# Kernel tuning notes

Measured on AMD Instinct MI355X. Metric: run time of the kernel, lower is better.

## Reference

```python
import jax, jax.numpy as jnp
import numpy as np

DIM = 192; HEADS = 6; WS = 7; RES = 56; SHIFT = 3
HEAD_DIM = DIM // HEADS
SCALE = HEAD_DIM ** -0.5
N = WS * WS
EPS = 1e-5

def _rel_pos_index():
    coords = np.stack(np.meshgrid(np.arange(WS), np.arange(WS), indexing='ij')).reshape(2, -1)
    rel = coords[:, :, None] - coords[:, None, :]  # [2,N,N]
    rel = rel.transpose(1, 2, 0)
    rel[:, :, 0] += WS - 1
    rel[:, :, 1] += WS - 1
    rel[:, :, 0] *= 2 * WS - 1
    return rel.sum(-1)  # [N,N]

def _attn_mask():
    img = np.zeros((RES, RES), dtype=np.float32)
    slices = (slice(0, -WS), slice(-WS, -SHIFT), slice(-SHIFT, None))
    cnt = 0
    for h in slices:
        for w in slices:
            img[h, w] = cnt; cnt += 1
    mw = img.reshape(RES // WS, WS, RES // WS, WS).transpose(0, 2, 1, 3).reshape(-1, N)  # [nW,N]
    diff = mw[:, None, :] - mw[:, :, None]
    return np.where(diff != 0, -100.0, 0.0).astype(np.float32)  # [nW,N,N]

REL_IDX = jnp.asarray(_rel_pos_index())
ATTN_MASK = jnp.asarray(_attn_mask())

def _ln(x, g, b):
    mu = x.mean(-1, keepdims=True)
    var = ((x - mu) ** 2).mean(-1, keepdims=True)
    return (x - mu) * jax.lax.rsqrt(var + EPS) * g + b

def setup_inputs() -> dict:
    key = jax.random.key(0)
    ks = jax.random.split(key, 8)
    d = {
        'x': jax.random.normal(ks[0], (32, RES * RES, DIM), jnp.float32),
        'norm1_g': jnp.ones((DIM,), jnp.float32), 'norm1_b': jnp.zeros((DIM,), jnp.float32),
        'qkv_w': jax.random.normal(ks[1], (DIM, 3 * DIM), jnp.float32) * 0.02,
        'qkv_b': jnp.zeros((3 * DIM,), jnp.float32),
        'proj_w': jax.random.normal(ks[2], (DIM, DIM), jnp.float32) * 0.02,
        'proj_b': jnp.zeros((DIM,), jnp.float32),
        'bias_table': jax.random.normal(ks[3], ((2 * WS - 1) ** 2, HEADS), jnp.float32) * 0.02,
        'norm2_g': jnp.ones((DIM,), jnp.float32), 'norm2_b': jnp.zeros((DIM,), jnp.float32),
        'fc1_w': jax.random.normal(ks[4], (DIM, 4 * DIM), jnp.float32) * 0.02,
        'fc1_b': jnp.zeros((4 * DIM,), jnp.float32),
        'fc2_w': jax.random.normal(ks[5], (4 * DIM, DIM), jnp.float32) * 0.02,
        'fc2_b': jnp.zeros((DIM,), jnp.float32),
    }
    return d

def reference(x, norm1_g, norm1_b, qkv_w, qkv_b, proj_w, proj_b, bias_table,
              norm2_g, norm2_b, fc1_w, fc1_b, fc2_w, fc2_b):
    B, L, C = x.shape
    H = W = RES
    shortcut = x
    h = _ln(x, norm1_g, norm1_b).reshape(B, H, W, C)
    # cyclic shift
    h = jnp.roll(h, (-SHIFT, -SHIFT), axis=(1, 2))
    # window partition -> [B*nW, N, C]
    nH = H // WS
    h = h.reshape(B, nH, WS, nH, WS, C).transpose(0, 1, 3, 2, 4, 5).reshape(-1, N, C)
    BW = h.shape[0]
    # windowed MHSA
    qkv = (h @ qkv_w + qkv_b).reshape(BW, N, 3, HEADS, HEAD_DIM)
    q, k, v = qkv[:, :, 0], qkv[:, :, 1], qkv[:, :, 2]  # [BW,N,h,hd]
    attn = jnp.einsum('bnhd,bmhd->bhnm', q, k) * SCALE  # [BW,h,N,N]
    bias = bias_table[REL_IDX.reshape(-1)].reshape(N, N, HEADS).transpose(2, 0, 1)
    attn = attn + bias[None]
    nW = ATTN_MASK.shape[0]
    attn = attn.reshape(BW // nW, nW, HEADS, N, N) + ATTN_MASK[None, :, None]
    attn = jax.nn.softmax(attn.reshape(BW, HEADS, N, N), axis=-1)
    h = jnp.einsum('bhnm,bmhd->bnhd', attn, v).reshape(BW, N, C)
    h = h @ proj_w + proj_b
    # window reverse
    h = h.reshape(B, nH, nH, WS, WS, C).transpose(0, 1, 3, 2, 4, 5).reshape(B, H, W, C)
    h = jnp.roll(h, (SHIFT, SHIFT), axis=(1, 2)).reshape(B, L, C)
    x = shortcut + h
    # MLP
    m = _ln(x, norm2_g, norm2_b)
    m = jax.nn.gelu(m @ fc1_w + fc1_b, approximate=False) @ fc2_w + fc2_b
    return x + m
```

## Files before the change

### kernel.cpp

```cpp
#include <hip/hip_runtime.h>
#include <hip/hip_bf16.h>
#include <math.h>

typedef __attribute__((ext_vector_type(8))) short bh8;
typedef __attribute__((ext_vector_type(4))) float fx4;

__device__ __forceinline__ fx4 mfma_bf16(bh8 a, bh8 b, fx4 c) {
    return __builtin_amdgcn_mfma_f32_16x16x32_bf16(a, b, c, 0, 0, 0);
}

__device__ __forceinline__ void gload16(const __hip_bfloat16* g, __hip_bfloat16* l) {
    __builtin_amdgcn_global_load_lds(
        (const __attribute__((address_space(1))) void*)g,
        (__attribute__((address_space(3))) void*)l,
        16, 0, 0);
}

__global__ __launch_bounds__(256)
void convw_k(const float* __restrict__ W, __hip_bfloat16* __restrict__ Wt, int K, int Nn)
{
    int idx = blockIdx.x * 256 + threadIdx.x;
    if (idx < K * Nn) {
        int k = idx / Nn, n = idx - k * Nn;
        Wt[(size_t)n * K + k] = __float2bfloat16(W[idx]);
    }
}

__global__ __launch_bounds__(256)
void ln1_gather_k(const float* __restrict__ x, const float* __restrict__ g,
                  const float* __restrict__ bia, __hip_bfloat16* __restrict__ xw)
{
    const int wave = threadIdx.x >> 6, lane = threadIdx.x & 63;
    const int t = blockIdx.x * 4 + wave;
    const int w = t / 49, n = t - w * 49;
    const int b = w >> 6, wrem = w & 63, wi = wrem >> 3, wj = wrem & 7;
    const int i = n / 7, j = n - i * 7;
    int sr = wi * 7 + i + 3; if (sr >= 56) sr -= 56;
    int sc = wj * 7 + j + 3; if (sc >= 56) sc -= 56;
    const float* xp = x + ((size_t)b * 3136 + sr * 56 + sc) * 192;
    float v0 = xp[lane], v1 = xp[lane + 64], v2 = xp[lane + 128];
    float s = v0 + v1 + v2;
    float q = v0 * v0 + v1 * v1 + v2 * v2;
    for (int off = 32; off > 0; off >>= 1) {
        s += __shfl_down(s, off, 64);
        q += __shfl_down(q, off, 64);
    }
    s = __shfl(s, 0, 64); q = __shfl(q, 0, 64);
    float mean = s * (1.0f / 192.0f);
    float var  = q * (1.0f / 192.0f) - mean * mean;
    float rstd = rsqrtf(var + 1e-5f);
    __hip_bfloat16* op = xw + (size_t)t * 192;
    op[lane]       = __float2bfloat16((v0 - mean) * rstd * g[lane]       + bia[lane]);
    op[lane + 64]  = __float2bfloat16((v1 - mean) * rstd * g[lane + 64]  + bia[lane + 64]);
    op[lane + 128] = __float2bfloat16((v2 - mean) * rstd * g[lane + 128] + bia[lane + 128]);
}

template<int MODE, int K, int NOUT>
__global__ __launch_bounds__(256)
void gemm2_k(const __hip_bfloat16* __restrict__ A,
             const __hip_bfloat16* __restrict__ Bt,
             const float* __restrict__ bias,
             const float* __restrict__ resid,
             void* __restrict__ outv)
{
    __shared__ __align__(16) __hip_bfloat16 As[128 * 32];
    __shared__ __align__(16) __hip_bfloat16 Bs[64 * 32];
    const int tid  = threadIdx.x;
    const int lane = tid & 63, wave = tid >> 6;
    const int quad = lane >> 4, l15 = lane & 15;
    const int m0 = blockIdx.x * 128, n0 = blockIdx.y * 64;

    const int arow = lane >> 2, acol = (lane & 3) * 8;
    const __hip_bfloat16* Ag0 = A  + (size_t)(m0 + wave * 32 + arow)      * K + acol;
    const __hip_bfloat16* Ag1 = A  + (size_t)(m0 + wave * 32 + 16 + arow) * K + acol;
    const __hip_bfloat16* Bg  = Bt + (size_t)(n0 + wave * 16 + arow)      * K + acol;
    __hip_bfloat16* Al0 = &As[(wave * 32)      * 32];
    __hip_bfloat16* Al1 = &As[(wave * 32 + 16) * 32];
    __hip_bfloat16* Bl  = &Bs[(wave * 16)      * 32];

    fx4 acc[2][4];
#pragma unroll
    for (int mi = 0; mi < 2; mi++)
#pragma unroll
        for (int ni = 0; ni < 4; ni++) acc[mi][ni] = {0.f, 0.f, 0.f, 0.f};

    for (int k0 = 0; k0 < K; k0 += 32) {
        gload16(Ag0 + k0, Al0);
        gload16(Ag1 + k0, Al1);
        gload16(Bg  + k0, Bl);
        __syncthreads();
        bh8 a0 = *(const bh8*)&As[(wave * 32 + l15)      * 32 + quad * 8];
        bh8 a1 = *(const bh8*)&As[(wave * 32 + 16 + l15) * 32 + quad * 8];
        bh8 b0 = *(const bh8*)&Bs[(0 * 16 + l15) * 32 + quad * 8];
        bh8 b1 = *(const bh8*)&Bs[(1 * 16 + l15) * 32 + quad * 8];
        bh8 b2 = *(const bh8*)&Bs[(2 * 16 + l15) * 32 + quad * 8];
        bh8 b3 = *(const bh8*)&Bs[(3 * 16 + l15) * 32 + quad * 8];
        acc[0][0] = mfma_bf16(a0, b0, acc[0][0]);
        acc[0][1] = mfma_bf16(a0, b1, acc[0][1]);
        acc[0][2] = mfma_bf16(a0, b2, acc[0][2]);
        acc[0][3] = mfma_bf16(a0, b3, acc[0][3]);
        acc[1][0] = mfma_bf16(a1, b0, acc[1][0]);
        acc[1][1] = mfma_bf16(a1, b1, acc[1][1]);
        acc[1][2] = mfma_bf16(a1, b2, acc[1][2]);
        acc[1][3] = mfma_bf16(a1, b3, acc[1][3]);
        __syncthreads();
    }

#pragma unroll
    for (int mi = 0; mi < 2; mi++)
#pragma unroll
    for (int ni = 0; ni < 4; ni++) {
        const int n = n0 + ni * 16 + l15;
        const float bn = bias[n];
#pragma unroll
        for (int r = 0; r < 4; r++) {
            const int m = m0 + wave * 32 + mi * 16 + quad * 4 + r;
            float v = acc[mi][ni][r] + bn;
            if (MODE == 0) {
                if (n < 192) v *= 0.17677669529663687f;
                ((__hip_bfloat16*)outv)[(size_t)m * NOUT + n] = __float2bfloat16(v);
            } else if (MODE == 2) {
                v = 0.5f * v * (1.0f + erff(v * 0.70710678118654752f));
                ((__hip_bfloat16*)outv)[(size_t)m * NOUT + n] = __float2bfloat16(v);
            } else {
                ((float*)outv)[(size_t)m * NOUT + n] = v + resid[(size_t)m * NOUT + n];
            }
        }
    }
}

__global__ __launch_bounds__(256)
void mlp_k(const __hip_bfloat16* __restrict__ A,
           const __hip_bfloat16* __restrict__ W1t,
           const __hip_bfloat16* __restrict__ W2t,
           const float* __restrict__ b1,
           const float* __restrict__ b2,
           float* __restrict__ out)
{
    __shared__ __align__(16) __hip_bfloat16 Xs[6][64][32];
    __shared__ __align__(16) __hip_bfloat16 W1s[6][64][32];
    __shared__ __align__(16) __hip_bfloat16 W2s[2][192][32];
    __shared__ __align__(16) __hip_bfloat16 Hs[2][64][32];

    const int tid  = threadIdx.x;
    const int lane = tid & 63, wave = tid >> 6;
    const int quad = lane >> 4, l15 = lane & 15;
    const int m0 = blockIdx.x * 64;
    const int arow = lane >> 2, acol = (lane & 3) * 8;

    const __hip_bfloat16* xg  = A   + (size_t)(m0 + wave * 16 + arow) * 192 + acol;
    const __hip_bfloat16* w1g = W1t + (size_t)(wave * 16 + arow) * 192 + acol;
    const __hip_bfloat16* w2g = W2t + (size_t)(wave * 48 + arow) * 768 + acol;

#pragma unroll
    for (int kc = 0; kc < 6; kc++) {
        gload16(xg  + kc * 32, &Xs[kc][wave * 16][0]);
        gload16(w1g + kc * 32, &W1s[kc][wave * 16][0]);
    }
#pragma unroll
    for (int i = 0; i < 3; i++)
#pragma unroll
        for (int hc = 0; hc < 2; hc++)
            gload16(w2g + (size_t)i * 16 * 768 + hc * 32, &W2s[hc][wave * 48 + i * 16][0]);
    __syncthreads();

    fx4 acc2[12];
#pragma unroll
    for (int nt = 0; nt < 12; nt++) acc2[nt] = {0.f, 0.f, 0.f, 0.f};

    for (int c = 0; c < 12; c++) {
        float b1v[4];
#pragma unroll
        for (int ni = 0; ni < 4; ni++) b1v[ni] = b1[c * 64 + ni * 16 + l15];

        fx4 acc1[4];
#pragma unroll
        for (int ni = 0; ni < 4; ni++) acc1[ni] = {0.f, 0.f, 0.f, 0.f};
#pragma unroll
        for (int kc = 0; kc < 6; kc++) {
            bh8 a = *(const bh8*)&Xs[kc][wave * 16 + l15][quad * 8];
#pragma unroll
            for (int ni = 0; ni < 4; ni++) {
                bh8 b = *(const bh8*)&W1s[kc][ni * 16 + l15][quad * 8];
                acc1[ni] = mfma_bf16(a, b, acc1[ni]);
            }
        }
#pragma unroll
        for (int ni = 0; ni < 4; ni++) {
#pragma unroll
            for (int r = 0; r < 4; r++) {
                float v = acc1[ni][r] + b1v[ni];
                v = 0.5f * v * (1.0f + erff(v * 0.70710678118654752f));
                Hs[ni >> 1][wave * 16 + quad * 4 + r][(ni & 1) * 16 + l15] = __float2bfloat16(v);
            }
        }
        asm volatile("s_waitcnt lgkmcnt(0)" ::: "memory");
        __builtin_amdgcn_sched_barrier(0);

#pragma unroll
        for (int hc = 0; hc < 2; hc++) {
            bh8 ap = *(const bh8*)&Hs[hc][wave * 16 + l15][quad * 8];
#pragma unroll
            for (int nt = 0; nt < 12; nt++) {
                bh8 b = *(const bh8*)&W2s[hc][nt * 16 + l15][quad * 8];
                acc2[nt] = mfma_bf16(ap, b, acc2[nt]);
            }
        }
        __syncthreads();
        if (c < 11) {
#pragma unroll
            for (int kc = 0; kc < 6; kc++)
                gload16(w1g + (size_t)(c + 1) * 64 * 192 + kc * 32, &W1s[kc][wave * 16][0]);
#pragma unroll
            for (int i = 0; i < 3; i++)
#pragma unroll
                for (int hc = 0; hc < 2; hc++)
                    gload16(w2g + (size_t)i * 16 * 768 + (c + 1) * 64 + hc * 32,
                            &W2s[hc][wave * 48 + i * 16][0]);
            __syncthreads();
        }
    }

#pragma unroll
    for (int nt = 0; nt < 12; nt++) {
        const int n = nt * 16 + l15;
        const float bn = b2[n];
#pragma unroll
        for (int r = 0; r < 4; r++) {
            const int m = m0 + wave * 16 + quad * 4 + r;
            out[(size_t)m * 192 + n] += acc2[nt][r] + bn;
        }
    }
}

__global__ __launch_bounds__(256)
void projln_k(const __hip_bfloat16* __restrict__ A,
              const __hip_bfloat16* __restrict__ Bt,
              const float* __restrict__ pb,
              const float* __restrict__ xresid,
              const float* __restrict__ g2,
              const float* __restrict__ b2,
              float* __restrict__ x1out,
              __hip_bfloat16* __restrict__ y2out)
{
    __shared__ __align__(16) __hip_bfloat16 As[64 * 32];
    __shared__ __align__(16) __hip_bfloat16 Bs[192 * 32];
    const int tid  = threadIdx.x;
    const int lane = tid & 63, wave = tid >> 6;
    const int quad = lane >> 4, l15 = lane & 15;
    const int m0 = blockIdx.x * 64;

    const int arow = lane >> 2, acol = (lane & 3) * 8;
    const __hip_bfloat16* Ag = A + (size_t)(m0 + wave * 16 + arow) * 192 + acol;
    __hip_bfloat16* Al = &As[(wave * 16) * 32];
    const __hip_bfloat16* Bg0 = Bt + (size_t)((wave + 0) * 16 + arow) * 192 + acol;
    const __hip_bfloat16* Bg1 = Bt + (size_t)((wave + 4) * 16 + arow) * 192 + acol;
    const __hip_bfloat16* Bg2 = Bt + (size_t)((wave + 8) * 16 + arow) * 192 + acol;
    __hip_bfloat16* Bl0 = &Bs[((wave + 0) * 16) * 32];
    __hip_bfloat16* Bl1 = &Bs[((wave + 4) * 16) * 32];
    __hip_bfloat16* Bl2 = &Bs[((wave + 8) * 16) * 32];

    fx4 acc[12];
#pragma unroll
    for (int ct = 0; ct < 12; ct++) acc[ct] = {0.f, 0.f, 0.f, 0.f};

    for (int k0 = 0; k0 < 192; k0 += 32) {
        gload16(Ag  + k0, Al);
        gload16(Bg0 + k0, Bl0);
        gload16(Bg1 + k0, Bl1);
        gload16(Bg2 + k0, Bl2);
        __syncthreads();
        bh8 a = *(const bh8*)&As[(wave * 16 + l15) * 32 + quad * 8];
#pragma unroll
        for (int ct = 0; ct < 12; ct++) {
            bh8 b = *(const bh8*)&Bs[(ct * 16 + l15) * 32 + quad * 8];
            acc[ct] = mfma_bf16(a, b, acc[ct]);
        }
        __syncthreads();
    }

#pragma unroll
    for (int r = 0; r < 4; r++) {
        const int row = m0 + wave * 16 + quad * 4 + r;
        float vv[12];
        float s = 0.f, q = 0.f;
#pragma unroll
        for (int ct = 0; ct < 12; ct++) {
            const int col = ct * 16 + l15;
            float v = acc[ct][r] + pb[col] + xresid[(size_t)row * 192 + col];
            vv[ct] = v;
            x1out[(size_t)row * 192 + col] = v;
            s += v;
            q += v * v;
        }
        s += __shfl_xor(s, 1, 64);  q += __shfl_xor(q, 1, 64);
        s += __shfl_xor(s, 2, 64);  q += __shfl_xor(q, 2, 64);
        s += __shfl_xor(s, 4, 64);  q += __shfl_xor(q, 4, 64);
        s += __shfl_xor(s, 8, 64);  q += __shfl_xor(q, 8, 64);
        float mean = s * (1.0f / 192.0f);
        float var  = q * (1.0f / 192.0f) - mean * mean;
        float rstd = rsqrtf(var + 1e-5f);
#pragma unroll
        for (int ct = 0; ct < 12; ct++) {
            const int col = ct * 16 + l15;
            float y = (vv[ct] - mean) * rstd * g2[col] + b2[col];
            y2out[(size_t)row * 192 + col] = __float2bfloat16(y);
        }
    }
}

__global__ __launch_bounds__(256)
void attn_k(const __hip_bfloat16* __restrict__ qkv,
            const float* __restrict__ bias_table,
            __hip_bfloat16* __restrict__ aout)
{
    __shared__ __align__(16) __hip_bfloat16 Qb[64 * 32];
    __shared__ __align__(16) __hip_bfloat16 Kb[64 * 32];
    __shared__ __align__(16) __hip_bfloat16 Vt[32 * 64];
    __shared__ __align__(16) __hip_bfloat16 Ps[64 * 72];
    __shared__ float bias_h[169];

    const int tid  = threadIdx.x;
    const int lane = tid & 63, wave = tid >> 6;
    const int quad = lane >> 4, l15 = lane & 15;
    const int w = blockIdx.x / 6, hd = blockIdx.x % 6;
    const int b = w >> 6, wrem = w & 63, wi = wrem >> 3, wj = wrem & 7;
    const size_t base = (size_t)w * 49 * 576 + hd * 32;

    if (tid < 169) bias_h[tid] = bias_table[tid * 6 + hd];

    bh8 z = {0, 0, 0, 0, 0, 0, 0, 0};
    {
        int row = tid >> 2, ch = (tid & 3) * 8;
        if (row < 49) {
            *(bh8*)&Qb[row * 32 + ch] = *(const bh8*)(qkv + base + (size_t)row * 576 + ch);
            *(bh8*)&Kb[row * 32 + ch] = *(const bh8*)(qkv + base + (size_t)row * 576 + 192 + ch);
        } else {
            *(bh8*)&Qb[row * 32 + ch] = z;
            *(bh8*)&Kb[row * 32 + ch] = z;
        }
        *(bh8*)&Vt[tid * 8] = z;
    }
    __syncthreads();
    for (int idx = tid; idx < 49 * 32; idx += 256) {
        int n = idx >> 5, d = idx & 31;
        Vt[d * 64 + n] = qkv[base + (size_t)n * 576 + 384 + d];
    }
    __syncthreads();

    fx4 zf = {0.f, 0.f, 0.f, 0.f};
    bh8 aq = *(const bh8*)&Qb[(wave * 16 + l15) * 32 + quad * 8];
    fx4 sarr[4];
#pragma unroll
    for (int ni = 0; ni < 4; ni++) {
        bh8 bk = *(const bh8*)&Kb[(ni * 16 + l15) * 32 + quad * 8];
        sarr[ni] = mfma_bf16(aq, bk, zf);
    }

    int iarr[4], ria[4], cia[4], mbi[4];
#pragma unroll
    for (int r = 0; r < 4; r++) {
        int i = wave * 16 + quad * 4 + r;
        int ri = i / 7, ci = i - ri * 7;
        iarr[r] = i; ria[r] = ri; cia[r] = ci;
        int ar = wi * 7 + ri, ac = wj * 7 + ci;
        int br = (ar < 49) ? 0 : ((ar < 53) ? 1 : 2);
        int bc = (ac < 49) ? 0 : ((ac < 53) ? 1 : 2);
        mbi[r] = br * 3 + bc;
    }
    float vals[4][4];
#pragma unroll
    for (int ni = 0; ni < 4; ni++) {
        int jcol = ni * 16 + l15;
        int rj = jcol / 7, cj = jcol - rj * 7;
        int ar = wi * 7 + rj, ac = wj * 7 + cj;
        int br = (ar < 49) ? 0 : ((ar < 53) ? 1 : 2);
        int bc = (ac < 49) ? 0 : ((ac < 53) ? 1 : 2);
        int mbj = br * 3 + bc;
#pragma unroll
        for (int r = 0; r < 4; r++) {
            float v;
            if (jcol >= 49)            v = -1e30f;
            else if (iarr[r] >= 49)    v = 0.0f;
            else {
                int bidx = (ria[r] - rj + 6) * 13 + (cia[r] - cj + 6);
                v = sarr[ni][r] + bias_h[bidx] + ((mbi[r] != mbj) ? -100.0f : 0.0f);
            }
            vals[ni][r] = v;
        }
    }
#pragma unroll
    for (int r = 0; r < 4; r++) {
        float mx = fmaxf(fmaxf(vals[0][r], vals[1][r]), fmaxf(vals[2][r], vals[3][r]));
        mx = fmaxf(mx, __shfl_xor(mx, 1, 64));
        mx = fmaxf(mx, __shfl_xor(mx, 2, 64));
        mx = fmaxf(mx, __shfl_xor(mx, 4, 64));
        mx = fmaxf(mx, __shfl_xor(mx, 8, 64));
        float e0 = __expf(vals[0][r] - mx);
        float e1 = __expf(vals[1][r] - mx);
        float e2 = __expf(vals[2][r] - mx);
        float e3 = __expf(vals[3][r] - mx);
        float sm = e0 + e1 + e2 + e3;
        sm += __shfl_xor(sm, 1, 64);
        sm += __shfl_xor(sm, 2, 64);
        sm += __shfl_xor(sm, 4, 64);
        sm += __shfl_xor(sm, 8, 64);
        float inv = 1.0f / sm;
        int prow = (wave * 16 + quad * 4 + r) * 72;
        Ps[prow + 0 * 16 + l15] = __float2bfloat16(e0 * inv);
        Ps[prow + 1 * 16 + l15] = __float2bfloat16(e1 * inv);
        Ps[prow + 2 * 16 + l15] = __float2bfloat16(e2 * inv);
        Ps[prow + 3 * 16 + l15] = __float2bfloat16(e3 * inv);
    }
    __syncthreads();

    fx4 o0 = zf, o1 = zf;
#pragma unroll
    for (int k0 = 0; k0 < 64; k0 += 32) {
        bh8 ap  = *(const bh8*)&Ps[(wave * 16 + l15) * 72 + k0 + quad * 8];
        bh8 bv0 = *(const bh8*)&Vt[(l15)      * 64 + k0 + quad * 8];
        bh8 bv1 = *(const bh8*)&Vt[(16 + l15) * 64 + k0 + quad * 8];
        o0 = mfma_bf16(ap, bv0, o0);
        o1 = mfma_bf16(ap, bv1, o1);
    }

#pragma unroll
    for (int r = 0; r < 4; r++) {
        int m = wave * 16 + quad * 4 + r;
        if (m < 49) {
            int i = m / 7, j2 = m - i * 7;
            int orow = wi * 7 + i + 3;  if (orow >= 56) orow -= 56;
            int ocol = wj * 7 + j2 + 3; if (ocol >= 56) ocol -= 56;
            size_t t = (size_t)b * 3136 + orow * 56 + ocol;
            aout[t * 192 + hd * 32 + l15]      = __float2bfloat16(o0[r]);
            aout[t * 192 + hd * 32 + 16 + l15] = __float2bfloat16(o1[r]);
        }
    }
}

extern "C" void kernel_launch(void* const* d_in, const int* in_sizes, int n_in,
                              void* d_out, int out_size, void* d_ws, size_t ws_size,
                              hipStream_t stream)
{
    const float* x      = (const float*)d_in[0];
    const float* n1g    = (const float*)d_in[1];
    const float* n1b    = (const float*)d_in[2];
    const float* qkv_w  = (const float*)d_in[3];
    const float* qkv_b  = (const float*)d_in[4];
    const float* proj_w = (const float*)d_in[5];
    const float* proj_b = (const float*)d_in[6];
    const float* btab   = (const float*)d_in[7];
    const float* n2g    = (const float*)d_in[8];
    const float* n2b    = (const float*)d_in[9];
    const float* fc1_w  = (const float*)d_in[10];
    const float* fc1_b  = (const float*)d_in[11];
    const float* fc2_w  = (const float*)d_in[12];
    const float* fc2_b  = (const float*)d_in[13];

    char* ws = (char*)d_ws;
    __hip_bfloat16* buf1    = (__hip_bfloat16*)(ws + 0);
    __hip_bfloat16* buf2    = (__hip_bfloat16*)(ws + 38535168);
    __hip_bfloat16* wt_qkv  = (__hip_bfloat16*)(ws + 192675840);
    __hip_bfloat16* wt_proj = (__hip_bfloat16*)(ws + 192897024);
    __hip_bfloat16* wt_fc1  = (__hip_bfloat16*)(ws + 192970752);
    __hip_bfloat16* wt_fc2  = (__hip_bfloat16*)(ws + 193265664);
    float*          x1      = (float*)d_out;

    convw_k<<<dim3(432), 256, 0, stream>>>(qkv_w, wt_qkv, 192, 576);
    convw_k<<<dim3(144), 256, 0, stream>>>(proj_w, wt_proj, 192, 192);
    convw_k<<<dim3(576), 256, 0, stream>>>(fc1_w, wt_fc1, 192, 768);
    convw_k<<<dim3(576), 256, 0, stream>>>(fc2_w, wt_fc2, 768, 192);

    ln1_gather_k<<<dim3(25088), 256, 0, stream>>>(x, n1g, n1b, buf1);

    gemm2_k<0, 192, 576><<<dim3(784, 9), 256, 0, stream>>>(buf1, wt_qkv, qkv_b, nullptr, buf2);

    attn_k<<<dim3(12288), 256, 0, stream>>>(buf2, btab, buf1);

    projln_k<<<dim3(1568), 256, 0, stream>>>(buf1, wt_proj, proj_b, x, n2g, n2b, x1, buf1);

    mlp_k<<<dim3(1568), 256, 0, stream>>>(buf1, wt_fc1, wt_fc2, fc1_b, fc2_b, x1);
}
```

Before: 511.1 us.

## Double-buffer MLP weight chunks, keep X in registers, use fast erf GELU

The fused MLP kernel now holds the input row tile in registers rather than LDS. It walks the hidden dimension in 24 chunks of 32 instead of 12 chunks of 64, with double-buffered W1/W2 staging so the next chunk's global-to-LDS loads overlap the current chunk's MFMAs, and it drops one barrier per iteration. The exact erff is replaced by an Abramowitz-Stegun polynomial erf built on fast rcp/exp, which cuts transcendental cost but adds an approximation error of about 1e-7 before bf16 rounding. The Hs buffer is padded to 40 columns to reduce LDS bank conflicts.

```diff
diff --git a/kernel.cpp b/kernel.cpp
--- a/kernel.cpp
+++ b/kernel.cpp
@@ -14,6 +14,15 @@
         (const __attribute__((address_space(1))) void*)g,
         (__attribute__((address_space(3))) void*)l,
         16, 0, 0);
+}
+
+__device__ __forceinline__ float fast_erf(float u) {
+    float au = fabsf(u);
+    float t  = __builtin_amdgcn_rcpf(1.0f + 0.3275911f * au);
+    float p  = ((((1.061405429f * t - 1.453152027f) * t + 1.421413741f) * t
+                 - 0.284496736f) * t + 0.254829592f) * t;
+    float e  = __expf(-u * u);
+    return copysignf(1.0f - p * e, u);
 }
 
 __global__ __launch_bounds__(256)
@@ -137,10 +146,9 @@
            const float* __restrict__ b2,
            float* __restrict__ out)
 {
-    __shared__ __align__(16) __hip_bfloat16 Xs[6][64][32];
-    __shared__ __align__(16) __hip_bfloat16 W1s[6][64][32];
+    __shared__ __align__(16) __hip_bfloat16 W1s[2][6][32][32];
     __shared__ __align__(16) __hip_bfloat16 W2s[2][192][32];
-    __shared__ __align__(16) __hip_bfloat16 Hs[2][64][32];
+    __shared__ __align__(16) __hip_bfloat16 Hs[64][40];
 
     const int tid  = threadIdx.x;
     const int lane = tid & 63, wave = tid >> 6;
@@ -148,77 +156,71 @@
     const int m0 = blockIdx.x * 64;
     const int arow = lane >> 2, acol = (lane & 3) * 8;
 
-    const __hip_bfloat16* xg  = A   + (size_t)(m0 + wave * 16 + arow) * 192 + acol;
-    const __hip_bfloat16* w1g = W1t + (size_t)(wave * 16 + arow) * 192 + acol;
-    const __hip_bfloat16* w2g = W2t + (size_t)(wave * 48 + arow) * 768 + acol;
-
-#pragma unroll
-    for (int kc = 0; kc < 6; kc++) {
-        gload16(xg  + kc * 32, &Xs[kc][wave * 16][0]);
-        gload16(w1g + kc * 32, &W1s[kc][wave * 16][0]);
-    }
-#pragma unroll
-    for (int i = 0; i < 3; i++)
-#pragma unroll
-        for (int hc = 0; hc < 2; hc++)
-            gload16(w2g + (size_t)i * 16 * 768 + hc * 32, &W2s[hc][wave * 48 + i * 16][0]);
+    bh8 xr[6];
+    const __hip_bfloat16* xg = A + (size_t)(m0 + wave * 16 + l15) * 192 + quad * 8;
+#pragma unroll
+    for (int kc = 0; kc < 6; kc++) xr[kc] = *(const bh8*)(xg + kc * 32);
+
+    auto stage = [&](int bf, int c) {
+#pragma unroll
+        for (int i = 0; i < 3; i++) {
+            const int g = wave * 3 + i;
+            const int kc = g >> 1, half = g & 1;
+            gload16(W1t + (size_t)(c * 32 + half * 16 + arow) * 192 + kc * 32 + acol,
+                    &W1s[bf][kc][half * 16][0]);
+            gload16(W2t + (size_t)(g * 16 + arow) * 768 + c * 32 + acol,
+                    &W2s[bf][g * 16][0]);
+        }
+    };
+
+    fx4 acc2[12];
+#pragma unroll
+    for (int nt = 0; nt < 12; nt++) acc2[nt] = {0.f, 0.f, 0.f, 0.f};
+
+    stage(0, 0);
     __syncthreads();
 
-    fx4 acc2[12];
-#pragma unroll
-    for (int nt = 0; nt < 12; nt++) acc2[nt] = {0.f, 0.f, 0.f, 0.f};
-
-    for (int c = 0; c < 12; c++) {
-        float b1v[4];
-#pragma unroll
-        for (int ni = 0; ni < 4; ni++) b1v[ni] = b1[c * 64 + ni * 16 + l15];
-
-        fx4 acc1[4];
-#pragma unroll
-        for (int ni = 0; ni < 4; ni++) acc1[ni] = {0.f, 0.f, 0.f, 0.f};
+    int cur = 0;
+    for (int c = 0; c < 24; c++) {
+        if (c < 23) stage(cur ^ 1, c + 1);
+
+        float b1v0 = b1[c * 32 + l15];
+        float b1v1 = b1[c * 32 + 16 + l15];
+
+        fx4 acc1[2];
+        acc1[0] = {0.f, 0.f, 0.f, 0.f};
+        acc1[1] = {0.f, 0.f, 0.f, 0.f};
 #pragma unroll
         for (int kc = 0; kc < 6; kc++) {
-            bh8 a = *(const bh8*)&Xs[kc][wave * 16 + l15][quad * 8];
-#pragma unroll
-            for (int ni = 0; ni < 4; ni++) {
-                bh8 b = *(const bh8*)&W1s[kc][ni * 16 + l15][quad * 8];
-                acc1[ni] = mfma_bf16(a, b, acc1[ni]);
+#pragma unroll
+            for (int ni = 0; ni < 2; ni++) {
+                bh8 b = *(const bh8*)&W1s[cur][kc][ni * 16 + l15][quad * 8];
+                acc1[ni] = mfma_bf16(xr[kc], b, acc1[ni]);
             }
         }
-#pragma unroll
-        for (int ni = 0; ni < 4; ni++) {
+
+#pragma unroll
+        for (int ni = 0; ni < 2; ni++) {
+            const float bb = ni ? b1v1 : b1v0;
 #pragma unroll
             for (int r = 0; r < 4; r++) {
-                float v = acc1[ni][r] + b1v[ni];
-                v = 0.5f * v * (1.0f + erff(v * 0.70710678118654752f));
-                Hs[ni >> 1][wave * 16 + quad * 4 + r][(ni & 1) * 16 + l15] = __float2bfloat16(v);
+                float v = acc1[ni][r] + bb;
+                float h = 0.5f * v * (1.0f + fast_erf(v * 0.70710678118654752f));
+                Hs[wave * 16 + quad * 4 + r][ni * 16 + l15] = __float2bfloat16(h);
             }
         }
         asm volatile("s_waitcnt lgkmcnt(0)" ::: "memory");
         __builtin_amdgcn_sched_barrier(0);
 
-#pragma unroll
-        for (int hc = 0; hc < 2; hc++) {
-            bh8 ap = *(const bh8*)&Hs[hc][wave * 16 + l15][quad * 8];
-#pragma unroll
-            for (int nt = 0; nt < 12; nt++) {
-                bh8 b = *(const bh8*)&W2s[hc][nt * 16 + l15][quad * 8];
-                acc2[nt] = mfma_bf16(ap, b, acc2[nt]);
-            }
-        }
+        bh8 ap = *(const bh8*)&Hs[wave * 16 + l15][quad * 8];
+#pragma unroll
+        for (int nt = 0; nt < 12; nt++) {
+            bh8 b = *(const bh8*)&W2s[cur][nt * 16 + l15][quad * 8];
+            acc2[nt] = mfma_bf16(ap, b, acc2[nt]);
+        }
+
         __syncthreads();
-        if (c < 11) {
-#pragma unroll
-            for (int kc = 0; kc < 6; kc++)
-                gload16(w1g + (size_t)(c + 1) * 64 * 192 + kc * 32, &W1s[kc][wave * 16][0]);
-#pragma unroll
-            for (int i = 0; i < 3; i++)
-#pragma unroll
-                for (int hc = 0; hc < 2; hc++)
-                    gload16(w2g + (size_t)i * 16 * 768 + (c + 1) * 64 + hc * 32,
-                            &W2s[hc][wave * 48 + i * 16][0]);
-            __syncthreads();
-        }
+        cur ^= 1;
     }
 
 #pragma unroll
```

Result: slower. 532.3 us (+4.1%).
